# Performance work log

Hardware: AMD Instinct MI355X
Metric: run time of the kernel (lower is better)

## Reference

```python
import jax, jax.numpy as jnp
import numpy as np

B, T, F = 8192, 336, 8
H = 20        # lstm_hidden_size
DENSE = 20
OUT = 1
N_LAYERS = 3


def _param(key, shape, scale):
    return jax.random.uniform(key, shape, jnp.float32, -scale, scale)


def setup_inputs() -> dict:
    key = jax.random.key(0)
    ks = jax.random.split(key, 32)
    s = 1.0 / np.sqrt(H)
    inp = {"x": jax.random.normal(ks[0], (B, T, F), jnp.float32)}
    k = 1
    for l in range(N_LAYERS):
        in_size = F if l == 0 else H
        inp[f"W_ih{l}"] = _param(ks[k], (4 * H, in_size), s); k += 1
        inp[f"W_hh{l}"] = _param(ks[k], (4 * H, H), s); k += 1
        inp[f"b_ih{l}"] = _param(ks[k], (4 * H,), s); k += 1
        inp[f"b_hh{l}"] = _param(ks[k], (4 * H,), s); k += 1
    inp["fc1_w"] = _param(ks[k], (DENSE, H), 1.0 / np.sqrt(H)); k += 1
    inp["fc1_b"] = _param(ks[k], (DENSE,), 1.0 / np.sqrt(H)); k += 1
    inp["fc2_w"] = _param(ks[k], (OUT, DENSE), 1.0 / np.sqrt(DENSE)); k += 1
    inp["fc2_b"] = _param(ks[k], (OUT,), 1.0 / np.sqrt(DENSE)); k += 1
    return inp


def lstm_layer(x, W_ih, W_hh, b_ih, b_hh):
    """PyTorch-convention LSTM over [B, T, in]; returns hidden sequence [B, T, H]."""
    b = x.shape[0]
    # Precompute input contribution for all timesteps in one GEMM: [B, T, 4H]
    xg = jnp.einsum('bti,gi->btg', x, W_ih) + b_ih + b_hh
    W_hh_T = W_hh.T  # [H, 4H]

    def step(carry, xt):
        h, c = carry
        gates = xt + h @ W_hh_T                      # [B, 4H], gate order i,f,g,o
        i, f, g, o = jnp.split(gates, 4, axis=-1)
        i = jax.nn.sigmoid(i)
        f = jax.nn.sigmoid(f)
        g = jnp.tanh(g)
        o = jax.nn.sigmoid(o)
        c = f * c + i * g
        h = o * jnp.tanh(c)
        return (h, c), h

    h0 = jnp.zeros((b, W_hh.shape[1]), x.dtype)
    c0 = jnp.zeros_like(h0)
    _, hs = jax.lax.scan(step, (h0, c0), jnp.swapaxes(xg, 0, 1))  # [T, B, H]
    return jnp.swapaxes(hs, 0, 1)


def reference(x, W_ih0, W_hh0, b_ih0, b_hh0, W_ih1, W_hh1, b_ih1, b_hh1,
              W_ih2, W_hh2, b_ih2, b_hh2, fc1_w, fc1_b, fc2_w, fc2_b):
    layers = [(W_ih0, W_hh0, b_ih0, b_hh0),
              (W_ih1, W_hh1, b_ih1, b_hh1),
              (W_ih2, W_hh2, b_ih2, b_hh2)]
    h = x
    for (wi, wh, bi, bh) in layers:
        h = lstm_layer(h, wi, wh, bi, bh)
    h = h[:, -1, :]                         # last timestep, [B, H]
    # dropout layers are identity at inference
    h = jax.nn.relu(h @ fc1_w.T + fc1_b)    # [B, DENSE]
    return h @ fc2_w.T + fc2_b              # [B, OUT]
```

## Files before the change

kernel.cpp:

```cpp
#include <hip/hip_runtime.h>


#define T_LEN 336
#define NJ 85

typedef _Float16 f16;
typedef _Float16 f16x4 __attribute__((ext_vector_type(4)));
typedef _Float16 f16x8 __attribute__((ext_vector_type(8)));
typedef float f32x4 __attribute__((ext_vector_type(4)));

#define MFMA(a, b, c) __builtin_amdgcn_mfma_f32_16x16x32_f16((a), (b), (c), 0, 0, 0)

#define SWZ1(n, c) ((c) ^ (((n) & 7) << 3))

__device__ __forceinline__ float sigm(float x) {
  return __builtin_amdgcn_rcpf(1.0f + __builtin_amdgcn_exp2f(-1.4426950408889634f * x));
}
__device__ __forceinline__ float tanh_fast(float x) {
  return 2.0f * __builtin_amdgcn_rcpf(1.0f + __builtin_amdgcn_exp2f(-2.8853900817779268f * x)) - 1.0f;
}

#define CELLS5(DI, DF, DG, DO, DL, HV, HL) {                                                \
  { float i_=sigm((DI)[0]), f_=sigm((DF)[0]), g_=tanh_fast((DG)[0]), o_=sigm((DO)[0]);      \
    c0 = f_*c0 + i_*g_; (HV)[0] = (f16)(o_*tanh_fast(c0)); }                                \
  { float i_=sigm((DI)[1]), f_=sigm((DF)[1]), g_=tanh_fast((DG)[1]), o_=sigm((DO)[1]);      \
    c1 = f_*c1 + i_*g_; (HV)[1] = (f16)(o_*tanh_fast(c1)); }                                \
  { float i_=sigm((DI)[2]), f_=sigm((DF)[2]), g_=tanh_fast((DG)[2]), o_=sigm((DO)[2]);      \
    c2 = f_*c2 + i_*g_; (HV)[2] = (f16)(o_*tanh_fast(c2)); }                                \
  { float i_=sigm((DI)[3]), f_=sigm((DF)[3]), g_=tanh_fast((DG)[3]), o_=sigm((DO)[3]);      \
    c3 = f_*c3 + i_*g_; (HV)[3] = (f16)(o_*tanh_fast(c3)); }                                \
  { float i_=sigm((DL)[0]), f_=sigm((DL)[1]), g_=tanh_fast((DL)[2]), o_=sigm((DL)[3]);      \
    cL = f_*cL + i_*g_; (HL) = (f16)(o_*tanh_fast(cL)); } }

#define MSTEP(BA, SRC, SELF, PUB) {                                                         \
  f16x8 bb = *(const f16x8*)&(SRC)[n * 64 + SWZ1(n, 32 + q * 8)];                           \
  f32x4 di = MFMA(Fb0, bb, MFMA(Fa0, (BA), Bi));                                            \
  f32x4 df = MFMA(Fb1, bb, MFMA(Fa1, (BA), Bf));                                            \
  f32x4 dg = MFMA(Fb2, bb, MFMA(Fa2, (BA), Bg));                                            \
  f32x4 dn = MFMA(Fb3, bb, MFMA(Fa3, (BA), Bo));                                            \
  f32x4 dl = MFMA(Fb4, bb, MFMA(Fa4, (BA), BL));                                            \
  f16x4 hv; f16 hl; CELLS5(di, df, dg, dn, dl, hv, hl)                                      \
  f16* ds_ = (SELF);                                                                        \
  *(f16x4*)&ds_[n * 64 + SWZ1(n, 32 + q * 4)] = hv;                                         \
  ds_[n * 64 + SWZ1(n, 48 + q)] = hl;                                                       \
  f16* dp_ = (PUB);                                                                         \
  if (dp_) { *(f16x4*)&dp_[n * 64 + SWZ1(n, q * 4)] = hv;                                   \
             dp_[n * 64 + SWZ1(n, 16 + q)] = hl; } }

#define L0S(S, D, PUB) {                                                                    \
  f16x8 b0 = *(const f16x8*)&zT0[S][n * 64 + SWZ1(n, q * 8)];                               \
  f32x4 di = MFMA(Fa0, b0, Bi), df = MFMA(Fa1, b0, Bf), dg = MFMA(Fa2, b0, Bg),             \
        dn = MFMA(Fa3, b0, Bo), dl = MFMA(Fa4, b0, BL);                                     \
  f16x4 hv; f16 hl; CELLS5(di, df, dg, dn, dl, hv, hl)                                      \
  *(f16x4*)&zT0[D][n * 64 + SWZ1(n, 8 + q * 4)] = hv;                                       \
  zT0[D][n * 64 + SWZ1(n, 24 + q)] = hl;                                                    \
  f16* dp_ = (PUB);                                                                         \
  *(f16x4*)&dp_[n * 64 + SWZ1(n, q * 4)] = hv;                                              \
  dp_[n * 64 + SWZ1(n, 16 + q)] = hl; }

__global__ __launch_bounds__(192, 2) void lstm3_ws_kernel(
    const float* __restrict__ x,
    const float* __restrict__ Wih0, const float* __restrict__ Whh0,
    const float* __restrict__ bih0, const float* __restrict__ bhh0,
    const float* __restrict__ Wih1, const float* __restrict__ Whh1,
    const float* __restrict__ bih1, const float* __restrict__ bhh1,
    const float* __restrict__ Wih2, const float* __restrict__ Whh2,
    const float* __restrict__ bih2, const float* __restrict__ bhh2,
    const float* __restrict__ fc1w, const float* __restrict__ fc1b,
    const float* __restrict__ fc2w, const float* __restrict__ fc2b,
    float* __restrict__ out)
{
  __shared__ __align__(16) f16 zT0[4][16 * 64];
  __shared__ __align__(16) f16 zT1[2][4][16 * 64];
  __shared__ __align__(16) f16 zT2[2][4][16 * 64];
  __shared__ __align__(16) float pbuf[64];

  const int tid  = threadIdx.x;
  const int w    = tid >> 6;
  const int lane = tid & 63;
  const int n = lane & 15;
  const int q = lane >> 4;

  {
    f16x8 zer;
#pragma unroll
    for (int j = 0; j < 8; ++j) zer[j] = (f16)0.f;
    for (int i = tid; i < 512; i += 192)  ((f16x8*)&zT0[0][0])[i] = zer;
    for (int i = tid; i < 1024; i += 192) ((f16x8*)&zT1[0][0][0])[i] = zer;
    for (int i = tid; i < 1024; i += 192) ((f16x8*)&zT2[0][0][0])[i] = zer;
  }
  __syncthreads();

  auto rowmap = [](int T, int m) { return T < 4 ? T * 20 + m : (m & 3) * 20 + 16 + (m >> 2); };

  f16x8 Fa0{}, Fa1{}, Fa2{}, Fa3{}, Fa4{};
  f16x8 Fb0{}, Fb1{}, Fb2{}, Fb3{}, Fb4{};
  f32x4 Bi{}, Bf{}, Bg{}, Bo{}, BL{};
  float c0 = 0.f, c1 = 0.f, c2 = 0.f, c3 = 0.f, cL = 0.f;

  if (w == 0) {
    auto gA0 = [&](int T) {
      int row = rowmap(T, n);
      f16x8 r;
#pragma unroll
      for (int j = 0; j < 8; ++j) {
        int k = q * 8 + j;
        float v = (k < 8) ? Wih0[row * 8 + k] : (k < 28 ? Whh0[row * 20 + k - 8] : 0.f);
        r[j] = (f16)v;
      }
      return r;
    };
    Fa0 = gA0(0); Fa1 = gA0(1); Fa2 = gA0(2); Fa3 = gA0(3); Fa4 = gA0(4);
    auto gB = [&](int T) {
      f32x4 r;
#pragma unroll
      for (int j = 0; j < 4; ++j) { int row = rowmap(T, q * 4 + j); r[j] = bih0[row] + bhh0[row]; }
      return r;
    };
    Bi = gB(0); Bf = gB(1); Bg = gB(2); Bo = gB(3); BL = gB(4);
  } else {
    const float* Wi = (w == 1) ? Wih1 : Wih2;
    const float* Wh = (w == 1) ? Whh1 : Whh2;
    const float* bi = (w == 1) ? bih1 : bih2;
    const float* bh = (w == 1) ? bhh1 : bhh2;
    auto gA = [&](int T, int c) {
      int row = rowmap(T, n);
      const float* W = c ? Wh : Wi;
      f16x8 r;
#pragma unroll
      for (int j = 0; j < 8; ++j) {
        int k = q * 8 + j;
        r[j] = (f16)((k < 20) ? W[row * 20 + k] : 0.f);
      }
      return r;
    };
    Fa0 = gA(0, 0); Fb0 = gA(0, 1);
    Fa1 = gA(1, 0); Fb1 = gA(1, 1);
    Fa2 = gA(2, 0); Fb2 = gA(2, 1);
    Fa3 = gA(3, 0); Fb3 = gA(3, 1);
    Fa4 = gA(4, 0); Fb4 = gA(4, 1);
    auto gB = [&](int T) {
      f32x4 r;
#pragma unroll
      for (int j = 0; j < 4; ++j) { int row = rowmap(T, q * 4 + j); r[j] = bi[row] + bh[row]; }
      return r;
    };
    Bi = gB(0); Bf = gB(1); Bg = gB(2); Bo = gB(3); BL = gB(4);
  }

  const float* xb = x + (size_t)(blockIdx.x * 16 + n) * (T_LEN * 8) + 4 * q;
  f32x4 xA{}, xB{};
  if (w == 0) {
    xA = *(const f32x4*)(xb);
    xB = *(const f32x4*)(xb + 16);
  }

#pragma unroll 1
  for (int j = 0; j <= NJ; ++j) {
    asm volatile("" ::: "memory");
    __builtin_amdgcn_s_setprio(1);
    const int wp = j & 1, rp = wp ^ 1;
    if (w == 0) {
      if (j <= 83) {
        f16x4 xh;
        xh[0] = (f16)xA[0]; xh[1] = (f16)xA[1]; xh[2] = (f16)xA[2]; xh[3] = (f16)xA[3];
        *(f16x4*)&zT0[q >> 1][n * 64 + SWZ1(n, 4 * (q & 1))] = xh;
        xh[0] = (f16)xB[0]; xh[1] = (f16)xB[1]; xh[2] = (f16)xB[2]; xh[3] = (f16)xB[3];
        *(f16x4*)&zT0[2 + (q >> 1)][n * 64 + SWZ1(n, 4 * (q & 1))] = xh;
        int g = (j + 1 > 83) ? 83 : j + 1;
        xA = *(const f32x4*)(xb + (size_t)(2 * g) * 16);
        xB = *(const f32x4*)(xb + (size_t)(2 * g + 1) * 16);
        f16* p1 = &zT1[wp][0][0];
        L0S(0, 1, p1 + 0 * 1024)
        L0S(1, 2, p1 + 1 * 1024)
        L0S(2, 3, p1 + 2 * 1024)
        L0S(3, 0, p1 + 3 * 1024)
      }
    } else if (w == 1) {
      if (j >= 1 && j <= 84) {
        f16* s1 = &zT1[rp][0][0];
        f16x8 ba0 = *(const f16x8*)&s1[0 * 1024 + n * 64 + SWZ1(n, q * 8)];
        f16x8 ba1 = *(const f16x8*)&s1[1 * 1024 + n * 64 + SWZ1(n, q * 8)];
        f16x8 ba2 = *(const f16x8*)&s1[2 * 1024 + n * 64 + SWZ1(n, q * 8)];
        f16x8 ba3 = *(const f16x8*)&s1[3 * 1024 + n * 64 + SWZ1(n, q * 8)];
        f16* p2 = &zT2[wp][0][0];
        MSTEP(ba0, s1 + 0 * 1024, s1 + 1 * 1024, p2 + 0 * 1024)
        MSTEP(ba1, s1 + 1 * 1024, s1 + 2 * 1024, p2 + 1 * 1024)
        MSTEP(ba2, s1 + 2 * 1024, s1 + 3 * 1024, p2 + 2 * 1024)
        MSTEP(ba3, s1 + 3 * 1024, &zT1[wp][0][0], p2 + 3 * 1024)
      }
    } else {
      if (j >= 2) {
        f16* s2 = &zT2[rp][0][0];
        f16x8 ca0 = *(const f16x8*)&s2[0 * 1024 + n * 64 + SWZ1(n, q * 8)];
        f16x8 ca1 = *(const f16x8*)&s2[1 * 1024 + n * 64 + SWZ1(n, q * 8)];
        f16x8 ca2 = *(const f16x8*)&s2[2 * 1024 + n * 64 + SWZ1(n, q * 8)];
        f16x8 ca3 = *(const f16x8*)&s2[3 * 1024 + n * 64 + SWZ1(n, q * 8)];
        MSTEP(ca0, s2 + 0 * 1024, s2 + 1 * 1024, (f16*)nullptr)
        MSTEP(ca1, s2 + 1 * 1024, s2 + 2 * 1024, (f16*)nullptr)
        MSTEP(ca2, s2 + 2 * 1024, s2 + 3 * 1024, (f16*)nullptr)
        MSTEP(ca3, s2 + 3 * 1024, &zT2[wp][0][0], (f16*)nullptr)
      }
    }
    __builtin_amdgcn_s_setprio(0);
    asm volatile("s_waitcnt lgkmcnt(0)\n\ts_barrier" ::: "memory");
  }

  if (w == 2) {
    const f16* hb = &zT2[1][0][0];
    f16x4 hv0 = *(const f16x4*)&hb[n * 64 + SWZ1(n, 32)];
    f16x4 hv1 = *(const f16x4*)&hb[n * 64 + SWZ1(n, 36)];
    f16x4 hv2 = *(const f16x4*)&hb[n * 64 + SWZ1(n, 40)];
    f16x4 hv3 = *(const f16x4*)&hb[n * 64 + SWZ1(n, 44)];
    f16x4 hv4 = *(const f16x4*)&hb[n * 64 + SWZ1(n, 48)];
    float p = 0.f;
#pragma unroll
    for (int i = 0; i < 5; ++i) {
      int d = q * 5 + i;
      const float* wr = fc1w + d * 20;
      float s = fc1b[d]
        + wr[0]  * (float)hv0[0] + wr[1]  * (float)hv0[1] + wr[2]  * (float)hv0[2] + wr[3]  * (float)hv0[3]
        + wr[4]  * (float)hv1[0] + wr[5]  * (float)hv1[1] + wr[6]  * (float)hv1[2] + wr[7]  * (float)hv1[3]
        + wr[8]  * (float)hv2[0] + wr[9]  * (float)hv2[1] + wr[10] * (float)hv2[2] + wr[11] * (float)hv2[3]
        + wr[12] * (float)hv3[0] + wr[13] * (float)hv3[1] + wr[14] * (float)hv3[2] + wr[15] * (float)hv3[3]
        + wr[16] * (float)hv4[0] + wr[17] * (float)hv4[1] + wr[18] * (float)hv4[2] + wr[19] * (float)hv4[3];
      p += fc2w[d] * fmaxf(s, 0.f);
    }
    pbuf[n * 4 + q] = p;
    if (q == 0) {
      f32x4 pv = *(const f32x4*)&pbuf[n * 4];
      out[blockIdx.x * 16 + n] = pv[0] + pv[1] + pv[2] + pv[3] + fc2b[0];
    }
  }
}

extern "C" void kernel_launch(void* const* d_in, const int* in_sizes, int n_in,
                              void* d_out, int out_size, void* d_ws, size_t ws_size,
                              hipStream_t stream) {
  const float* x    = (const float*)d_in[0];
  const float* Wih0 = (const float*)d_in[1];
  const float* Whh0 = (const float*)d_in[2];
  const float* bih0 = (const float*)d_in[3];
  const float* bhh0 = (const float*)d_in[4];
  const float* Wih1 = (const float*)d_in[5];
  const float* Whh1 = (const float*)d_in[6];
  const float* bih1 = (const float*)d_in[7];
  const float* bhh1 = (const float*)d_in[8];
  const float* Wih2 = (const float*)d_in[9];
  const float* Whh2 = (const float*)d_in[10];
  const float* bih2 = (const float*)d_in[11];
  const float* bhh2 = (const float*)d_in[12];
  const float* fc1w = (const float*)d_in[13];
  const float* fc1b = (const float*)d_in[14];
  const float* fc2w = (const float*)d_in[15];
  const float* fc2b = (const float*)d_in[16];
  float* out = (float*)d_out;

  hipLaunchKernelGGL(lstm3_ws_kernel, dim3(8192 / 16), dim3(192), 0, stream,
                     x, Wih0, Whh0, bih0, bhh0,
                     Wih1, Whh1, bih1, bhh1,
                     Wih2, Whh2, bih2, bhh2,
                     fc1w, fc1b, fc2w, fc2b, out);
}
```

Before: 396.5 us.

## Keep recurrent hidden state in registers via bpermute and prescale gate weights

Layers 1 and 2 now carry their own hidden state between sub-steps in registers and rebuild the MFMA B operand with ds_bpermute cross-lane shuffles. This replaces the LDS store and reload of the self-recurrent h. Separately, the gate weights and biases are prescaled by -log2(e) (or -2·log2(e) for the g gate), so the activations skip one multiply each. The prescaled weights are stored in fp16, which slightly changes rounding. The bpermute path adds eight LDS-pipe ops per sub-step in place of one store and one load. The final hidden state is written back to LDS before the FC head.

After: 387.5 us. 1.02x faster.

```diff
diff --git a/kernel.cpp b/kernel.cpp
--- a/kernel.cpp
+++ b/kernel.cpp
@@ -8,41 +8,60 @@
 typedef _Float16 f16x4 __attribute__((ext_vector_type(4)));
 typedef _Float16 f16x8 __attribute__((ext_vector_type(8)));
 typedef float f32x4 __attribute__((ext_vector_type(4)));
+typedef int i32x2 __attribute__((ext_vector_type(2)));
+typedef int i32x4 __attribute__((ext_vector_type(4)));
 
 #define MFMA(a, b, c) __builtin_amdgcn_mfma_f32_16x16x32_f16((a), (b), (c), 0, 0, 0)
 
 #define SWZ1(n, c) ((c) ^ (((n) & 7) << 3))
 
-__device__ __forceinline__ float sigm(float x) {
-  return __builtin_amdgcn_rcpf(1.0f + __builtin_amdgcn_exp2f(-1.4426950408889634f * x));
+#define KS1 1.4426950408889634f
+#define KS2 2.8853900817779268f
+
+__device__ __forceinline__ float sigm_p(float y) {
+  return __builtin_amdgcn_rcpf(1.0f + __builtin_amdgcn_exp2f(y));
+}
+__device__ __forceinline__ float tanh_p(float y) {
+  return 2.0f * __builtin_amdgcn_rcpf(1.0f + __builtin_amdgcn_exp2f(y)) - 1.0f;
 }
 __device__ __forceinline__ float tanh_fast(float x) {
-  return 2.0f * __builtin_amdgcn_rcpf(1.0f + __builtin_amdgcn_exp2f(-2.8853900817779268f * x)) - 1.0f;
+  return 2.0f * __builtin_amdgcn_rcpf(1.0f + __builtin_amdgcn_exp2f(-KS2 * x)) - 1.0f;
 }
 
 #define CELLS5(DI, DF, DG, DO, DL, HV, HL) {                                                \
-  { float i_=sigm((DI)[0]), f_=sigm((DF)[0]), g_=tanh_fast((DG)[0]), o_=sigm((DO)[0]);      \
+  { float i_=sigm_p((DI)[0]), f_=sigm_p((DF)[0]), g_=tanh_p((DG)[0]), o_=sigm_p((DO)[0]);   \
     c0 = f_*c0 + i_*g_; (HV)[0] = (f16)(o_*tanh_fast(c0)); }                                \
-  { float i_=sigm((DI)[1]), f_=sigm((DF)[1]), g_=tanh_fast((DG)[1]), o_=sigm((DO)[1]);      \
+  { float i_=sigm_p((DI)[1]), f_=sigm_p((DF)[1]), g_=tanh_p((DG)[1]), o_=sigm_p((DO)[1]);   \
     c1 = f_*c1 + i_*g_; (HV)[1] = (f16)(o_*tanh_fast(c1)); }                                \
-  { float i_=sigm((DI)[2]), f_=sigm((DF)[2]), g_=tanh_fast((DG)[2]), o_=sigm((DO)[2]);      \
+  { float i_=sigm_p((DI)[2]), f_=sigm_p((DF)[2]), g_=tanh_p((DG)[2]), o_=sigm_p((DO)[2]);   \
     c2 = f_*c2 + i_*g_; (HV)[2] = (f16)(o_*tanh_fast(c2)); }                                \
-  { float i_=sigm((DI)[3]), f_=sigm((DF)[3]), g_=tanh_fast((DG)[3]), o_=sigm((DO)[3]);      \
+  { float i_=sigm_p((DI)[3]), f_=sigm_p((DF)[3]), g_=tanh_p((DG)[3]), o_=sigm_p((DO)[3]);   \
     c3 = f_*c3 + i_*g_; (HV)[3] = (f16)(o_*tanh_fast(c3)); }                                \
-  { float i_=sigm((DL)[0]), f_=sigm((DL)[1]), g_=tanh_fast((DL)[2]), o_=sigm((DL)[3]);      \
+  { float i_=sigm_p((DL)[0]), f_=sigm_p((DL)[1]), g_=tanh_p((DL)[2]), o_=sigm_p((DL)[3]);   \
     cL = f_*cL + i_*g_; (HL) = (f16)(o_*tanh_fast(cL)); } }
 
-#define MSTEP(BA, SRC, SELF, PUB) {                                                         \
-  f16x8 bb = *(const f16x8*)&(SRC)[n * 64 + SWZ1(n, 32 + q * 8)];                           \
+#define MSTEP_REG(BA, PUB) {                                                                \
+  i32x2 _lo = __builtin_bit_cast(i32x2, hvS);                                               \
+  int _hlu = (int)(unsigned)__builtin_bit_cast(unsigned short, hlS);                        \
+  int _b0 = __builtin_amdgcn_ds_bpermute(adrA, _lo.x);                                      \
+  int _b1 = __builtin_amdgcn_ds_bpermute(adrA, _lo.y);                                      \
+  int _b2 = __builtin_amdgcn_ds_bpermute(adrB, _lo.x);                                      \
+  int _b3 = __builtin_amdgcn_ds_bpermute(adrB, _lo.y);                                      \
+  int _hA = __builtin_amdgcn_ds_bpermute(adr0, _hlu);                                       \
+  int _hB = __builtin_amdgcn_ds_bpermute(adr1, _hlu);                                       \
+  int _hC = __builtin_amdgcn_ds_bpermute(adr2, _hlu);                                       \
+  int _hD = __builtin_amdgcn_ds_bpermute(adr3, _hlu);                                       \
+  int _w0 = (q < 2) ? _b0 : ((_hA & 0xffff) | (_hB << 16));                                 \
+  int _w1 = (q < 2) ? _b1 : ((_hC & 0xffff) | (_hD << 16));                                 \
+  i32x4 _bbi = { _w0, _w1, _b2, _b3 };                                                      \
+  f16x8 bb = __builtin_bit_cast(f16x8, _bbi);                                               \
   f32x4 di = MFMA(Fb0, bb, MFMA(Fa0, (BA), Bi));                                            \
   f32x4 df = MFMA(Fb1, bb, MFMA(Fa1, (BA), Bf));                                            \
   f32x4 dg = MFMA(Fb2, bb, MFMA(Fa2, (BA), Bg));                                            \
   f32x4 dn = MFMA(Fb3, bb, MFMA(Fa3, (BA), Bo));                                            \
   f32x4 dl = MFMA(Fb4, bb, MFMA(Fa4, (BA), BL));                                            \
   f16x4 hv; f16 hl; CELLS5(di, df, dg, dn, dl, hv, hl)                                      \
-  f16* ds_ = (SELF);                                                                        \
-  *(f16x4*)&ds_[n * 64 + SWZ1(n, 32 + q * 4)] = hv;                                         \
-  ds_[n * 64 + SWZ1(n, 48 + q)] = hl;                                                       \
+  hvS = hv; hlS = hl;                                                                       \
   f16* dp_ = (PUB);                                                                         \
   if (dp_) { *(f16x4*)&dp_[n * 64 + SWZ1(n, q * 4)] = hv;                                   \
              dp_[n * 64 + SWZ1(n, 16 + q)] = hl; } }
@@ -81,6 +100,10 @@
   const int n = lane & 15;
   const int q = lane >> 4;
 
+  const int adrA = 4 * (n + 32 * (q & 1));
+  const int adrB = 4 * (n + 16 + 32 * (q & 1));
+  const int adr0 = 4 * n, adr1 = 4 * (n + 16), adr2 = 4 * (n + 32), adr3 = 4 * (n + 48);
+
   {
     f16x8 zer;
 #pragma unroll
@@ -92,21 +115,28 @@
   __syncthreads();
 
   auto rowmap = [](int T, int m) { return T < 4 ? T * 20 + m : (m & 3) * 20 + 16 + (m >> 2); };
+  auto gscale = [](int T, int m) {
+    int g = (T < 4) ? T : (m & 3);
+    return (g == 2) ? -KS2 : -KS1;
+  };
 
   f16x8 Fa0{}, Fa1{}, Fa2{}, Fa3{}, Fa4{};
   f16x8 Fb0{}, Fb1{}, Fb2{}, Fb3{}, Fb4{};
   f32x4 Bi{}, Bf{}, Bg{}, Bo{}, BL{};
   float c0 = 0.f, c1 = 0.f, c2 = 0.f, c3 = 0.f, cL = 0.f;
+  f16x4 hvS{};
+  f16 hlS = (f16)0.f;
 
   if (w == 0) {
     auto gA0 = [&](int T) {
       int row = rowmap(T, n);
+      float sc = gscale(T, n);
       f16x8 r;
 #pragma unroll
       for (int j = 0; j < 8; ++j) {
         int k = q * 8 + j;
         float v = (k < 8) ? Wih0[row * 8 + k] : (k < 28 ? Whh0[row * 20 + k - 8] : 0.f);
-        r[j] = (f16)v;
+        r[j] = (f16)(sc * v);
       }
       return r;
     };
@@ -114,7 +144,11 @@
     auto gB = [&](int T) {
       f32x4 r;
 #pragma unroll
-      for (int j = 0; j < 4; ++j) { int row = rowmap(T, q * 4 + j); r[j] = bih0[row] + bhh0[row]; }
+      for (int j = 0; j < 4; ++j) {
+        int m = q * 4 + j;
+        int row = rowmap(T, m);
+        r[j] = gscale(T, m) * (bih0[row] + bhh0[row]);
+      }
       return r;
     };
     Bi = gB(0); Bf = gB(1); Bg = gB(2); Bo = gB(3); BL = gB(4);
@@ -125,12 +159,13 @@
     const float* bh = (w == 1) ? bhh1 : bhh2;
     auto gA = [&](int T, int c) {
       int row = rowmap(T, n);
+      float sc = gscale(T, n);
       const float* W = c ? Wh : Wi;
       f16x8 r;
 #pragma unroll
       for (int j = 0; j < 8; ++j) {
         int k = q * 8 + j;
-        r[j] = (f16)((k < 20) ? W[row * 20 + k] : 0.f);
+        r[j] = (f16)((k < 20) ? sc * W[row * 20 + k] : 0.f);
       }
       return r;
     };
@@ -142,7 +177,11 @@
     auto gB = [&](int T) {
       f32x4 r;
 #pragma unroll
-      for (int j = 0; j < 4; ++j) { int row = rowmap(T, q * 4 + j); r[j] = bi[row] + bh[row]; }
+      for (int j = 0; j < 4; ++j) {
+        int m = q * 4 + j;
+        int row = rowmap(T, m);
+        r[j] = gscale(T, m) * (bi[row] + bh[row]);
+      }
       return r;
     };
     Bi = gB(0); Bf = gB(1); Bg = gB(2); Bo = gB(3); BL = gB(4);
@@ -184,10 +223,10 @@
         f16x8 ba2 = *(const f16x8*)&s1[2 * 1024 + n * 64 + SWZ1(n, q * 8)];
         f16x8 ba3 = *(const f16x8*)&s1[3 * 1024 + n * 64 + SWZ1(n, q * 8)];
         f16* p2 = &zT2[wp][0][0];
-        MSTEP(ba0, s1 + 0 * 1024, s1 + 1 * 1024, p2 + 0 * 1024)
-        MSTEP(ba1, s1 + 1 * 1024, s1 + 2 * 1024, p2 + 1 * 1024)
-        MSTEP(ba2, s1 + 2 * 1024, s1 + 3 * 1024, p2 + 2 * 1024)
-        MSTEP(ba3, s1 + 3 * 1024, &zT1[wp][0][0], p2 + 3 * 1024)
+        MSTEP_REG(ba0, p2 + 0 * 1024)
+        MSTEP_REG(ba1, p2 + 1 * 1024)
+        MSTEP_REG(ba2, p2 + 2 * 1024)
+        MSTEP_REG(ba3, p2 + 3 * 1024)
       }
     } else {
       if (j >= 2) {
@@ -196,10 +235,10 @@
         f16x8 ca1 = *(const f16x8*)&s2[1 * 1024 + n * 64 + SWZ1(n, q * 8)];
         f16x8 ca2 = *(const f16x8*)&s2[2 * 1024 + n * 64 + SWZ1(n, q * 8)];
         f16x8 ca3 = *(const f16x8*)&s2[3 * 1024 + n * 64 + SWZ1(n, q * 8)];
-        MSTEP(ca0, s2 + 0 * 1024, s2 + 1 * 1024, (f16*)nullptr)
-        MSTEP(ca1, s2 + 1 * 1024, s2 + 2 * 1024, (f16*)nullptr)
-        MSTEP(ca2, s2 + 2 * 1024, s2 + 3 * 1024, (f16*)nullptr)
-        MSTEP(ca3, s2 + 3 * 1024, &zT2[wp][0][0], (f16*)nullptr)
+        MSTEP_REG(ca0, (f16*)nullptr)
+        MSTEP_REG(ca1, (f16*)nullptr)
+        MSTEP_REG(ca2, (f16*)nullptr)
+        MSTEP_REG(ca3, (f16*)nullptr)
       }
     }
     __builtin_amdgcn_s_setprio(0);
@@ -207,6 +246,9 @@
   }
 
   if (w == 2) {
+    *(f16x4*)&zT2[1][0][n * 64 + SWZ1(n, 32 + q * 4)] = hvS;
+    zT2[1][0][n * 64 + SWZ1(n, 48 + q)] = hlS;
+    asm volatile("s_waitcnt lgkmcnt(0)" ::: "memory");
     const f16* hb = &zT2[1][0][0];
     f16x4 hv0 = *(const f16x4*)&hb[n * 64 + SWZ1(n, 32)];
     f16x4 hv1 = *(const f16x4*)&hb[n * 64 + SWZ1(n, 36)];
```
